# Optimization experiments

Hardware: AMD Instinct MI355X
Metric: run time of the kernel (lower is better)

The kernel has to match this reference:

```python
import jax, jax.numpy as jnp
import numpy as np

HEAD_SIZE = 16  # matches init_kwargs head_size


def _rope_angles(seq_len, half_dim, base=10000.0):
    # standard RoPE frequencies, matches typical precompute_pos_cis
    freqs = 1.0 / (base ** (np.arange(0, half_dim, dtype=np.float32) / half_dim))
    t = np.arange(seq_len, dtype=np.float32)
    ang = np.outer(t, freqs)  # (S, half_dim)
    return jnp.asarray(np.cos(ang)), jnp.asarray(np.sin(ang))


def setup_inputs() -> dict:
    key = jax.random.key(0)
    ks = jax.random.split(key, 10)
    B, S, D = 2, 2048, 1024
    hd = D // HEAD_SIZE
    pos_cos, pos_sin = _rope_angles(S, hd // 2)
    w = lambda k: jax.random.normal(k, (D, D), jnp.float32) * 0.02
    b = lambda k: jax.random.normal(k, (D,), jnp.float32) * 0.02
    return {
        "x": jax.random.normal(ks[0], (B, S, D), jnp.float32),
        "pos_cos": pos_cos,
        "pos_sin": pos_sin,
        "wq_w": w(ks[1]), "wq_b": b(ks[2]),
        "wk_w": w(ks[3]), "wk_b": b(ks[4]),
        "wv_w": w(ks[5]), "wv_b": b(ks[6]),
        "wo_w": w(ks[7]), "wo_b": b(ks[8]),
    }


def _apply_rope(t, cos, sin):
    # t: (B, S, H, hd); cos/sin: (S, hd//2) -> broadcast (1, S, 1, hd//2)
    B, S, H, hd = t.shape
    tr = t.reshape(B, S, H, hd // 2, 2)
    a, b = tr[..., 0], tr[..., 1]
    c = cos[None, :, None, :]
    s = sin[None, :, None, :]
    # complex multiply (a + ib) * (c + is)
    out_r = a * c - b * s
    out_i = a * s + b * c
    return jnp.stack([out_r, out_i], axis=-1).reshape(B, S, H, hd)


def reference(x, pos_cos, pos_sin, wq_w, wq_b, wk_w, wk_b, wv_w, wv_b, wo_w, wo_b):
    B, S, D = x.shape
    H = HEAD_SIZE
    hd = D // H
    q = (x @ wq_w.T + wq_b).reshape(B, S, H, hd)
    k = (x @ wk_w.T + wk_b).reshape(B, S, H, hd)
    v = (x @ wv_w.T + wv_b).reshape(B, S, H, hd)
    q = _apply_rope(q, pos_cos, pos_sin)
    k = _apply_rope(k, pos_cos, pos_sin)
    scale = 1.0 / jnp.sqrt(jnp.asarray(hd, x.dtype))
    scores = jnp.einsum('bshd,bthd->bhst', q, k) * scale  # (B,H,S,S)
    causal = jnp.tril(jnp.ones((S, S), bool))
    scores = jnp.where(causal[None, None], scores, jnp.asarray(-jnp.inf, scores.dtype))
    probs = jax.nn.softmax(scores, axis=-1)
    out = jnp.einsum('bhst,bthd->bshd', probs, v).reshape(B, S, D)
    return out @ wo_w.T + wo_b
```

## Files before the change

### kernel.cpp

```cpp
#include <hip/hip_runtime.h>
#include <stdint.h>
#include <stddef.h>


typedef __bf16 bf16x8 __attribute__((ext_vector_type(8)));
typedef float  f32x4  __attribute__((ext_vector_type(4)));

__device__ __forceinline__ unsigned short f2b(float f) {
  union { float f; uint32_t u; } v; v.f = f;
  uint32_t u = v.u;
  return (unsigned short)((u + 0x7FFFu + ((u >> 16) & 1u)) >> 16);
}

__device__ __forceinline__ void async16(const void* g, void* l) {
  __builtin_amdgcn_global_load_lds(
      (const __attribute__((address_space(1))) void*)g,
      (__attribute__((address_space(3))) void*)l, 16, 0, 0);
}

__global__ void cast_x_tiled_kernel(const float* __restrict__ in,
                                    unsigned short* __restrict__ out) {
  int i = blockIdx.x * blockDim.x + threadIdx.x;
  const int L  = i & 1023;
  const int kt = (i >> 10) & 15;
  const int pn = i >> 14;
  const int row = pn * 128 + ((L >> 7) << 4) + (L & 15);
  const int k0  = kt * 64 + ((L >> 4) & 7) * 8;
  const float4* src = (const float4*)(in + (size_t)row * 1024 + k0);
  float4 a = src[0], b = src[1];
  uint4 pk;
  pk.x = (uint32_t)f2b(a.x) | ((uint32_t)f2b(a.y) << 16);
  pk.y = (uint32_t)f2b(a.z) | ((uint32_t)f2b(a.w) << 16);
  pk.z = (uint32_t)f2b(b.x) | ((uint32_t)f2b(b.y) << 16);
  pk.w = (uint32_t)f2b(b.z) | ((uint32_t)f2b(b.w) << 16);
  *(uint4*)(out + (size_t)i * 8) = pk;
}

__global__ void cast_w_tiled_kernel(const float* __restrict__ wq,
                                    const float* __restrict__ wk,
                                    const float* __restrict__ wv,
                                    unsigned short* __restrict__ out) {
  int i = blockIdx.x * blockDim.x + threadIdx.x;
  const int mat = i >> 17;
  const int rem = i & 131071;
  const int L  = rem & 1023;
  const int kt = (rem >> 10) & 15;
  const int pn = rem >> 14;
  const float* src = (mat == 0) ? wq : (mat == 1) ? wk : wv;
  const int row = pn * 128 + ((L >> 7) << 4) + (L & 15);
  const int k0  = kt * 64 + ((L >> 4) & 7) * 8;
  const float4* s = (const float4*)(src + (size_t)row * 1024 + k0);
  float4 a = s[0], b = s[1];
  uint4 pk;
  pk.x = (uint32_t)f2b(a.x) | ((uint32_t)f2b(a.y) << 16);
  pk.y = (uint32_t)f2b(a.z) | ((uint32_t)f2b(a.w) << 16);
  pk.z = (uint32_t)f2b(b.x) | ((uint32_t)f2b(b.y) << 16);
  pk.w = (uint32_t)f2b(b.z) | ((uint32_t)f2b(b.w) << 16);
  *(uint4*)(out + (size_t)i * 8) = pk;
}

__global__ void cast_kernel(const float* __restrict__ in,
                            unsigned short* __restrict__ out, int n4) {
  int i = blockIdx.x * blockDim.x + threadIdx.x;
  if (i >= n4) return;
  float4 v = ((const float4*)in)[i];
  ushort4 o;
  o.x = f2b(v.x); o.y = f2b(v.y); o.z = f2b(v.z); o.w = f2b(v.w);
  ((ushort4*)out)[i] = o;
}

__global__ __launch_bounds__(256, 3) void qkv_gemm_kernel(
    const unsigned short* __restrict__ A,
    const unsigned short* __restrict__ W,
    const float* __restrict__ biasq, const float* __restrict__ biask,
    const float* __restrict__ biasv,
    const float* __restrict__ cp, const float* __restrict__ sp,
    unsigned short* __restrict__ qo,
    unsigned short* __restrict__ ko,
    unsigned short* __restrict__ vo)
{
  const int tid  = threadIdx.x;
  const int w    = tid >> 6, l = tid & 63;
  const int lm   = l & 15,  quad = l >> 4;
  const int nblk = blockIdx.x;
  const int m0   = blockIdx.y * 128;
  const int wm   = (w >> 1) * 64, wn = (w & 1) * 64;

  const unsigned short* At = A + (size_t)blockIdx.y * 16 * 8192;
  const unsigned short* Wt = W + (size_t)nblk * 16 * 8192;

  const f32x4 fzero = {0.f, 0.f, 0.f, 0.f};
  f32x4 acc[4][4];
#pragma unroll
  for (int i = 0; i < 4; ++i)
#pragma unroll
    for (int j = 0; j < 4; ++j) acc[i][j] = fzero;

  bf16x8 pA[4], pB[4], qA[4], qB[4];

#define QKV_LOADH(DA, DB, T, KK)                                              \
  {                                                                           \
    const unsigned short* Ab_ = At + (size_t)(T) * 8192;                      \
    const unsigned short* Wb_ = Wt + (size_t)(T) * 8192;                      \
    _Pragma("unroll")                                                         \
    for (int i = 0; i < 4; ++i)                                               \
      DA[i] = *(const bf16x8*)(Ab_ +                                          \
          (size_t)((((w >> 1) * 4 + i) * 128 + (KK) * 64 + l)) * 8);          \
    _Pragma("unroll")                                                         \
    for (int j = 0; j < 4; ++j)                                               \
      DB[j] = *(const bf16x8*)(Wb_ +                                          \
          (size_t)((((w & 1) * 4 + j) * 128 + (KK) * 64 + l)) * 8);           \
  }

#define QKV_MFMAH(SA, SB)                                                     \
  _Pragma("unroll")                                                           \
  for (int i = 0; i < 4; ++i)                                                 \
    _Pragma("unroll")                                                         \
    for (int j = 0; j < 4; ++j)                                               \
      acc[i][j] = __builtin_amdgcn_mfma_f32_16x16x32_bf16(SA[i], SB[j],       \
                                                          acc[i][j], 0, 0, 0);

  QKV_LOADH(pA, pB, 0, 0);
#pragma unroll 1
  for (int t = 0; t < 16; ++t) {
    QKV_LOADH(qA, qB, t, 1);
    QKV_MFMAH(pA, pB);
    if (t < 15) QKV_LOADH(pA, pB, t + 1, 0);
    QKV_MFMAH(qA, qB);
  }
#undef QKV_LOADH
#undef QKV_MFMAH

  const int which = nblk >> 3;
  const int n0    = (nblk & 7) * 128;
  const float* bias = (which == 0) ? biasq : (which == 1) ? biask : biasv;
#pragma unroll
  for (int i = 0; i < 4; ++i) {
#pragma unroll
    for (int j = 0; j < 4; ++j) {
      const int n = n0 + wn + j * 16 + lm;
      const float bval = bias[n];
      const int h = n >> 6, d = n & 63;
      float vals[4];
#pragma unroll
      for (int r = 0; r < 4; ++r) {
        const int m = m0 + wm + i * 16 + quad * 4 + r;
        const int srow = m & 2047;
        float val = acc[i][j][r] + bval;
        if (which != 2) {
          const float c  = cp[srow * 32 + (d >> 1)];
          const float sn = sp[srow * 32 + (d >> 1)];
          const float part = __shfl_xor(val, 1, 64);
          val = (d & 1) ? (part * sn + val * c) : (val * c - part * sn);
        }
        vals[r] = val;
      }
      const int mbase = m0 + wm + i * 16 + quad * 4;
      const int b = mbase >> 11, s0 = mbase & 2047;
      const int bh = (b << 4) + h;
      if (which == 0) {
#pragma unroll
        for (int r = 0; r < 4; ++r)
          qo[((size_t)bh * 2048 + s0 + r) * 64 + d] = f2b(vals[r]);
      } else if (which == 1) {
#pragma unroll
        for (int r = 0; r < 4; ++r) {
          const int s = s0 + r;
          ko[((size_t)bh * 32 + (s >> 6)) * 4096 +
             (size_t)(((d >> 3) * 64 + (s & 63))) * 8 + (d & 7)] = f2b(vals[r]);
        }
      } else {
        uint32_t w0 = (uint32_t)f2b(vals[0]) | ((uint32_t)f2b(vals[1]) << 16);
        uint32_t w1 = (uint32_t)f2b(vals[2]) | ((uint32_t)f2b(vals[3]) << 16);
        uint2 pk; pk.x = w0; pk.y = w1;
        *(uint2*)(vo + ((size_t)bh * 32 + (s0 >> 6)) * 4096 +
                  (size_t)((((s0 & 63) >> 3) * 64 + d)) * 8 + (s0 & 7)) = pk;
      }
    }
  }
}

__global__ __launch_bounds__(256, 4) void flash_kernel(
    const unsigned short* __restrict__ Q,
    const unsigned short* __restrict__ K,
    const unsigned short* __restrict__ VT,
    unsigned short* __restrict__ O)
{
  constexpr int PSTRIDE = 72;
  __shared__ unsigned short Ps[64 * PSTRIDE];
  const int tid = threadIdx.x;
  const int w = tid >> 6, l = tid & 63, lm = l & 15, quad = l >> 4;
  const int bh = blockIdx.x, qt = 31 - (int)blockIdx.y;
  const int row0 = qt * 64 + w * 16;

  bf16x8 aq[2];
#pragma unroll
  for (int kc = 0; kc < 2; ++kc)
    aq[kc] = *(const bf16x8*)(Q + ((size_t)bh * 2048 + row0 + lm) * 64 + kc * 32 + quad * 8);

  const f32x4 fzero = {0.f, 0.f, 0.f, 0.f};
  f32x4 Oacc[4];
#pragma unroll
  for (int jo = 0; jo < 4; ++jo) Oacc[jo] = fzero;
  float m_i = -1e30f, l_i = 0.f;

  const int nkv = qt + 1;

#pragma unroll 1
  for (int kt = 0; kt < nkv - 1; ++kt) {
    const size_t tbase = ((size_t)bh * 32 + kt) * 4096;
    bf16x8 kf[2][4], vf[2][4];
#pragma unroll
    for (int kc = 0; kc < 2; ++kc)
#pragma unroll
      for (int tb = 0; tb < 4; ++tb) {
        const size_t off = tbase + (size_t)(((kc * 4 + quad) * 64 + tb * 16 + lm)) * 8;
        kf[kc][tb] = *(const bf16x8*)(K + off);
        vf[kc][tb] = *(const bf16x8*)(VT + off);
      }
    f32x4 Sc[4];
#pragma unroll
    for (int tb = 0; tb < 4; ++tb) Sc[tb] = fzero;
#pragma unroll
    for (int kc = 0; kc < 2; ++kc)
#pragma unroll
      for (int tb = 0; tb < 4; ++tb)
        Sc[tb] = __builtin_amdgcn_mfma_f32_16x16x32_bf16(kf[kc][tb], aq[kc], Sc[tb], 0, 0, 0);

    float mx = -1e30f;
#pragma unroll
    for (int tb = 0; tb < 4; ++tb)
#pragma unroll
      for (int r = 0; r < 4; ++r) {
        float s = Sc[tb][r] * 0.125f;
        Sc[tb][r] = s;
        mx = fmaxf(mx, s);
      }
    mx = fmaxf(mx, __shfl_xor(mx, 16, 64));
    mx = fmaxf(mx, __shfl_xor(mx, 32, 64));

    const bool skip = (bool)__all(mx - m_i <= 8.0f);
    float alpha = 1.f;
    if (!skip) {
      const float mnew = fmaxf(m_i, mx);
      alpha = __expf(m_i - mnew);
      m_i = mnew;
    }
    const float mref = m_i;

    float ps = 0.f;
#pragma unroll
    for (int tb = 0; tb < 4; ++tb) {
      float p0 = __expf(Sc[tb][0] - mref), p1 = __expf(Sc[tb][1] - mref);
      float p2 = __expf(Sc[tb][2] - mref), p3 = __expf(Sc[tb][3] - mref);
      ps += (p0 + p1) + (p2 + p3);
      uint2 pk;
      pk.x = (uint32_t)f2b(p0) | ((uint32_t)f2b(p1) << 16);
      pk.y = (uint32_t)f2b(p2) | ((uint32_t)f2b(p3) << 16);
      *(uint2*)(Ps + (size_t)(w * 16 + lm) * PSTRIDE + tb * 16 + quad * 4) = pk;
    }
    ps += __shfl_xor(ps, 16, 64);
    ps += __shfl_xor(ps, 32, 64);
    if (skip) {
      l_i += ps;
    } else {
      l_i = l_i * alpha + ps;
      float af4[4];
#pragma unroll
      for (int r = 0; r < 4; ++r) af4[r] = __shfl(alpha, quad * 4 + r, 64);
#pragma unroll
      for (int jo = 0; jo < 4; ++jo)
#pragma unroll
        for (int r = 0; r < 4; ++r) Oacc[jo][r] *= af4[r];
    }

#pragma unroll
    for (int kc = 0; kc < 2; ++kc) {
      bf16x8 ap = *(const bf16x8*)(Ps + (size_t)(w * 16 + lm) * PSTRIDE + kc * 32 + quad * 8);
#pragma unroll
      for (int jo = 0; jo < 4; ++jo)
        Oacc[jo] = __builtin_amdgcn_mfma_f32_16x16x32_bf16(ap, vf[kc][jo], Oacc[jo], 0, 0, 0);
    }
  }

  {
    const size_t tbase = ((size_t)bh * 32 + qt) * 4096;
    bf16x8 kf[2][4], vf[2][4];
#pragma unroll
    for (int kc = 0; kc < 2; ++kc)
#pragma unroll
      for (int tb = 0; tb < 4; ++tb) {
        const size_t off = tbase + (size_t)(((kc * 4 + quad) * 64 + tb * 16 + lm)) * 8;
        kf[kc][tb] = *(const bf16x8*)(K + off);
        vf[kc][tb] = *(const bf16x8*)(VT + off);
      }
    f32x4 Sc[4];
#pragma unroll
    for (int tb = 0; tb < 4; ++tb) Sc[tb] = fzero;
#pragma unroll
    for (int kc = 0; kc < 2; ++kc)
#pragma unroll
      for (int tb = 0; tb < 4; ++tb)
        Sc[tb] = __builtin_amdgcn_mfma_f32_16x16x32_bf16(kf[kc][tb], aq[kc], Sc[tb], 0, 0, 0);

    const int mrel = w * 16 + lm;
    float mx = -1e30f;
#pragma unroll
    for (int tb = 0; tb < 4; ++tb)
#pragma unroll
      for (int r = 0; r < 4; ++r) {
        float s = Sc[tb][r] * 0.125f;
        if (tb * 16 + quad * 4 + r > mrel) s = -1e30f;
        Sc[tb][r] = s;
        mx = fmaxf(mx, s);
      }
    mx = fmaxf(mx, __shfl_xor(mx, 16, 64));
    mx = fmaxf(mx, __shfl_xor(mx, 32, 64));
    const float mnew  = fmaxf(m_i, mx);
    const float alpha = __expf(m_i - mnew);
    m_i = mnew;

    float ps = 0.f;
#pragma unroll
    for (int tb = 0; tb < 4; ++tb) {
      float p0 = __expf(Sc[tb][0] - mnew), p1 = __expf(Sc[tb][1] - mnew);
      float p2 = __expf(Sc[tb][2] - mnew), p3 = __expf(Sc[tb][3] - mnew);
      ps += (p0 + p1) + (p2 + p3);
      uint2 pk;
      pk.x = (uint32_t)f2b(p0) | ((uint32_t)f2b(p1) << 16);
      pk.y = (uint32_t)f2b(p2) | ((uint32_t)f2b(p3) << 16);
      *(uint2*)(Ps + (size_t)(w * 16 + lm) * PSTRIDE + tb * 16 + quad * 4) = pk;
    }
    ps += __shfl_xor(ps, 16, 64);
    ps += __shfl_xor(ps, 32, 64);
    l_i = l_i * alpha + ps;

    float af4[4];
#pragma unroll
    for (int r = 0; r < 4; ++r) af4[r] = __shfl(alpha, quad * 4 + r, 64);
#pragma unroll
    for (int jo = 0; jo < 4; ++jo)
#pragma unroll
      for (int r = 0; r < 4; ++r) Oacc[jo][r] *= af4[r];

#pragma unroll
    for (int kc = 0; kc < 2; ++kc) {
      bf16x8 ap = *(const bf16x8*)(Ps + (size_t)(w * 16 + lm) * PSTRIDE + kc * 32 + quad * 8);
#pragma unroll
      for (int jo = 0; jo < 4; ++jo)
        Oacc[jo] = __builtin_amdgcn_mfma_f32_16x16x32_bf16(ap, vf[kc][jo], Oacc[jo], 0, 0, 0);
    }
  }

  float lf[4];
#pragma unroll
  for (int r = 0; r < 4; ++r) lf[r] = 1.0f / __shfl(l_i, quad * 4 + r, 64);
  const int b = bh >> 4, h = bh & 15;
#pragma unroll
  for (int jo = 0; jo < 4; ++jo)
#pragma unroll
    for (int r = 0; r < 4; ++r) {
      const int s   = row0 + quad * 4 + r;
      const int col = h * 64 + jo * 16 + lm;
      O[((size_t)b * 2048 + s) * 1024 + col] = f2b(Oacc[jo][r] * lf[r]);
    }
}

__global__ __launch_bounds__(256) void oproj_gemm_kernel(
    const unsigned short* __restrict__ A,
    const unsigned short* __restrict__ W,
    const float* __restrict__ bias,
    float* __restrict__ out)
{
  __shared__ unsigned short As[64 * 64];
  __shared__ unsigned short Bs[128 * 64];
  const int tid = threadIdx.x;
  const int w = tid >> 6, l = tid & 63;
  const int lm = l & 15, quad = l >> 4;
  const int m0 = blockIdx.y * 64;
  const int n0 = blockIdx.x * 128;

  const f32x4 fzero = {0.f, 0.f, 0.f, 0.f};
  f32x4 acc[4][2];
#pragma unroll
  for (int i = 0; i < 4; ++i)
#pragma unroll
    for (int j = 0; j < 2; ++j) acc[i][j] = fzero;

  for (int k0 = 0; k0 < 1024; k0 += 64) {
    __syncthreads();
#pragma unroll
    for (int q = 0; q < 2; ++q) {
      const int row = w * 16 + lm;
      const int kc  = quad + 4 * q;
      async16(A + (size_t)(m0 + row) * 1024 + k0 + kc * 8,
              As + ((size_t)w * 128 + 64 * q) * 8);
    }
#pragma unroll
    for (int q = 0; q < 4; ++q) {
      const int row = w * 16 + lm + (q & 1) * 64;
      const int kc  = quad + 4 * (q >> 1);
      async16(W + (size_t)(n0 + row) * 1024 + k0 + kc * 8,
              Bs + ((size_t)(w + 4 * (q & 1)) * 128 + 64 * (q >> 1)) * 8);
    }
    __syncthreads();
#pragma unroll
    for (int kk = 0; kk < 2; ++kk) {
      bf16x8 af[4], bfc[2];
#pragma unroll
      for (int i = 0; i < 4; ++i)
        af[i] = *(const bf16x8*)(As + (size_t)((i * 128 + kk * 64 + l)) * 8);
#pragma unroll
      for (int j = 0; j < 2; ++j)
        bfc[j] = *(const bf16x8*)(Bs + (size_t)(((w * 2 + j) * 128 + kk * 64 + l)) * 8);
#pragma unroll
      for (int i = 0; i < 4; ++i)
#pragma unroll
        for (int j = 0; j < 2; ++j)
          acc[i][j] = __builtin_amdgcn_mfma_f32_16x16x32_bf16(af[i], bfc[j], acc[i][j], 0, 0, 0);
    }
  }

#pragma unroll
  for (int i = 0; i < 4; ++i) {
#pragma unroll
    for (int j = 0; j < 2; ++j) {
      const int n = n0 + w * 32 + j * 16 + lm;
      const float bval = bias[n];
#pragma unroll
      for (int r = 0; r < 4; ++r) {
        const int m = m0 + i * 16 + quad * 4 + r;
        out[(size_t)m * 1024 + n] = acc[i][j][r] + bval;
      }
    }
  }
}

extern "C" void kernel_launch(void* const* d_in, const int* in_sizes, int n_in,
                              void* d_out, int out_size, void* d_ws, size_t ws_size,
                              hipStream_t stream) {
  (void)in_sizes; (void)n_in; (void)out_size; (void)ws_size;
  const float* x  = (const float*)d_in[0];
  const float* cp = (const float*)d_in[1];
  const float* sp = (const float*)d_in[2];
  const float* wq = (const float*)d_in[3];
  const float* bq = (const float*)d_in[4];
  const float* wk = (const float*)d_in[5];
  const float* bk = (const float*)d_in[6];
  const float* wv = (const float*)d_in[7];
  const float* bv = (const float*)d_in[8];
  const float* wo = (const float*)d_in[9];
  const float* bo = (const float*)d_in[10];
  float* out = (float*)d_out;

  unsigned short* xbf  = (unsigned short*)d_ws;
  unsigned short* wqkv = xbf  + (size_t)4 * 1024 * 1024;
  unsigned short* wobf = wqkv + (size_t)3 * 1024 * 1024;
  unsigned short* qbf  = wobf + (size_t)1 * 1024 * 1024;
  unsigned short* kbf  = qbf  + (size_t)4 * 1024 * 1024;
  unsigned short* vbf  = kbf  + (size_t)4 * 1024 * 1024;
  unsigned short* obf  = vbf  + (size_t)4 * 1024 * 1024;

  hipLaunchKernelGGL(cast_x_tiled_kernel, dim3(2048), dim3(256), 0, stream, x, xbf);
  hipLaunchKernelGGL(cast_w_tiled_kernel, dim3(1536), dim3(256), 0, stream,
                     wq, wk, wv, wqkv);
  hipLaunchKernelGGL(cast_kernel, dim3(1024), dim3(256), 0, stream, wo, wobf, 262144);

  hipLaunchKernelGGL(qkv_gemm_kernel, dim3(24, 32), dim3(256), 0, stream,
                     xbf, wqkv, bq, bk, bv, cp, sp, qbf, kbf, vbf);
  hipLaunchKernelGGL(flash_kernel, dim3(32, 32), dim3(256), 0, stream,
                     qbf, kbf, vbf, obf);
  hipLaunchKernelGGL(oproj_gemm_kernel, dim3(8, 64), dim3(256), 0, stream,
                     obf, wobf, bo, out);
}
```

Measured before the change: 209.8 us.

## Fuse casts into one kernel and feed o-proj from pre-tiled layouts via registers

The three cast kernels are merged into one launch that writes x and all four weight matrices in an MFMA-fragment tiled layout. The flash kernel now stores its output in the same tiled layout, so the output-projection GEMM can load fragments straight from global memory into registers. That GEMM drops LDS staging and barriers and double-buffers its register loads across k-steps. The intent is fewer launches and no LDS round-trips or syncs, at the cost of the flash kernel's scattered 2-byte stores and loads that reach global memory without LDS reuse.

```diff
diff --git a/kernel.cpp b/kernel.cpp
--- a/kernel.cpp
+++ b/kernel.cpp
@@ -12,41 +12,33 @@
   return (unsigned short)((u + 0x7FFFu + ((u >> 16) & 1u)) >> 16);
 }
 
-__device__ __forceinline__ void async16(const void* g, void* l) {
-  __builtin_amdgcn_global_load_lds(
-      (const __attribute__((address_space(1))) void*)g,
-      (__attribute__((address_space(3))) void*)l, 16, 0, 0);
-}
-
-__global__ void cast_x_tiled_kernel(const float* __restrict__ in,
-                                    unsigned short* __restrict__ out) {
+__global__ void cast_all_kernel(const float* __restrict__ x,
+                                const float* __restrict__ wq,
+                                const float* __restrict__ wk,
+                                const float* __restrict__ wv,
+                                const float* __restrict__ wo,
+                                unsigned short* __restrict__ xbf,
+                                unsigned short* __restrict__ wqkv,
+                                unsigned short* __restrict__ wobf) {
   int i = blockIdx.x * blockDim.x + threadIdx.x;
-  const int L  = i & 1023;
-  const int kt = (i >> 10) & 15;
-  const int pn = i >> 14;
-  const int row = pn * 128 + ((L >> 7) << 4) + (L & 15);
-  const int k0  = kt * 64 + ((L >> 4) & 7) * 8;
-  const float4* src = (const float4*)(in + (size_t)row * 1024 + k0);
-  float4 a = src[0], b = src[1];
-  uint4 pk;
-  pk.x = (uint32_t)f2b(a.x) | ((uint32_t)f2b(a.y) << 16);
-  pk.y = (uint32_t)f2b(a.z) | ((uint32_t)f2b(a.w) << 16);
-  pk.z = (uint32_t)f2b(b.x) | ((uint32_t)f2b(b.y) << 16);
-  pk.w = (uint32_t)f2b(b.z) | ((uint32_t)f2b(b.w) << 16);
-  *(uint4*)(out + (size_t)i * 8) = pk;
-}
-
-__global__ void cast_w_tiled_kernel(const float* __restrict__ wq,
-                                    const float* __restrict__ wk,
-                                    const float* __restrict__ wv,
-                                    unsigned short* __restrict__ out) {
-  int i = blockIdx.x * blockDim.x + threadIdx.x;
-  const int mat = i >> 17;
-  const int rem = i & 131071;
-  const int L  = rem & 1023;
-  const int kt = (rem >> 10) & 15;
-  const int pn = rem >> 14;
-  const float* src = (mat == 0) ? wq : (mat == 1) ? wk : wv;
+  const float* src;
+  unsigned short* dst;
+  int rem;
+  if (i < 524288) {
+    src = x; dst = xbf; rem = i;
+  } else if (i < 917504) {
+    rem = i - 524288;
+    const int mat = rem >> 17;
+    src = (mat == 0) ? wq : (mat == 1) ? wk : wv;
+    dst = wqkv;
+  } else {
+    rem = i - 917504;
+    src = wo; dst = wobf;
+  }
+  const int inmat = (i < 524288) ? rem : (i < 917504) ? (rem & 131071) : rem;
+  const int L  = inmat & 1023;
+  const int kt = (inmat >> 10) & 15;
+  const int pn = inmat >> 14;
   const int row = pn * 128 + ((L >> 7) << 4) + (L & 15);
   const int k0  = kt * 64 + ((L >> 4) & 7) * 8;
   const float4* s = (const float4*)(src + (size_t)row * 1024 + k0);
@@ -56,17 +48,10 @@
   pk.y = (uint32_t)f2b(a.z) | ((uint32_t)f2b(a.w) << 16);
   pk.z = (uint32_t)f2b(b.x) | ((uint32_t)f2b(b.y) << 16);
   pk.w = (uint32_t)f2b(b.z) | ((uint32_t)f2b(b.w) << 16);
-  *(uint4*)(out + (size_t)i * 8) = pk;
-}
-
-__global__ void cast_kernel(const float* __restrict__ in,
-                            unsigned short* __restrict__ out, int n4) {
-  int i = blockIdx.x * blockDim.x + threadIdx.x;
-  if (i >= n4) return;
-  float4 v = ((const float4*)in)[i];
-  ushort4 o;
-  o.x = f2b(v.x); o.y = f2b(v.y); o.z = f2b(v.z); o.w = f2b(v.w);
-  ((ushort4*)out)[i] = o;
+  const size_t oidx = (i < 524288) ? (size_t)rem
+                    : (i < 917504) ? (size_t)rem
+                    : (size_t)rem;
+  *(uint4*)(dst + oidx * 8) = pk;
 }
 
 __global__ __launch_bounds__(256, 3) void qkv_gemm_kernel(
@@ -356,29 +341,32 @@
 #pragma unroll
   for (int r = 0; r < 4; ++r) lf[r] = 1.0f / __shfl(l_i, quad * 4 + r, 64);
   const int b = bh >> 4, h = bh & 15;
-#pragma unroll
-  for (int jo = 0; jo < 4; ++jo)
-#pragma unroll
-    for (int r = 0; r < 4; ++r) {
-      const int s   = row0 + quad * 4 + r;
-      const int col = h * 64 + jo * 16 + lm;
-      O[((size_t)b * 2048 + s) * 1024 + col] = f2b(Oacc[jo][r] * lf[r]);
-    }
-}
-
-__global__ __launch_bounds__(256) void oproj_gemm_kernel(
+  const size_t obase = ((size_t)((b * 16 + (qt >> 1)) * 16 + h)) * 8192;
+  const int Lbase = ((qt & 1) * 4 + w) * 128 + quad * 4;
+#pragma unroll
+  for (int jo = 0; jo < 4; ++jo) {
+    const int Ljo = Lbase + (jo * 2 + (lm >> 3)) * 16;
+#pragma unroll
+    for (int r = 0; r < 4; ++r)
+      O[obase + (size_t)(Ljo + r) * 8 + (lm & 7)] = f2b(Oacc[jo][r] * lf[r]);
+  }
+}
+
+__global__ __launch_bounds__(256, 2) void oproj_gemm_kernel(
     const unsigned short* __restrict__ A,
     const unsigned short* __restrict__ W,
     const float* __restrict__ bias,
     float* __restrict__ out)
 {
-  __shared__ unsigned short As[64 * 64];
-  __shared__ unsigned short Bs[128 * 64];
   const int tid = threadIdx.x;
   const int w = tid >> 6, l = tid & 63;
   const int lm = l & 15, quad = l >> 4;
+  const int nblk = blockIdx.x;
   const int m0 = blockIdx.y * 64;
-  const int n0 = blockIdx.x * 128;
+  const int half = blockIdx.y & 1;
+
+  const unsigned short* At = A + (size_t)(blockIdx.y >> 1) * 16 * 8192;
+  const unsigned short* Wt = W + (size_t)nblk * 16 * 8192;
 
   const f32x4 fzero = {0.f, 0.f, 0.f, 0.f};
   f32x4 acc[4][2];
@@ -387,45 +375,46 @@
 #pragma unroll
     for (int j = 0; j < 2; ++j) acc[i][j] = fzero;
 
-  for (int k0 = 0; k0 < 1024; k0 += 64) {
-    __syncthreads();
-#pragma unroll
-    for (int q = 0; q < 2; ++q) {
-      const int row = w * 16 + lm;
-      const int kc  = quad + 4 * q;
-      async16(A + (size_t)(m0 + row) * 1024 + k0 + kc * 8,
-              As + ((size_t)w * 128 + 64 * q) * 8);
-    }
-#pragma unroll
-    for (int q = 0; q < 4; ++q) {
-      const int row = w * 16 + lm + (q & 1) * 64;
-      const int kc  = quad + 4 * (q >> 1);
-      async16(W + (size_t)(n0 + row) * 1024 + k0 + kc * 8,
-              Bs + ((size_t)(w + 4 * (q & 1)) * 128 + 64 * (q >> 1)) * 8);
-    }
-    __syncthreads();
-#pragma unroll
-    for (int kk = 0; kk < 2; ++kk) {
-      bf16x8 af[4], bfc[2];
-#pragma unroll
-      for (int i = 0; i < 4; ++i)
-        af[i] = *(const bf16x8*)(As + (size_t)((i * 128 + kk * 64 + l)) * 8);
-#pragma unroll
-      for (int j = 0; j < 2; ++j)
-        bfc[j] = *(const bf16x8*)(Bs + (size_t)(((w * 2 + j) * 128 + kk * 64 + l)) * 8);
-#pragma unroll
-      for (int i = 0; i < 4; ++i)
-#pragma unroll
-        for (int j = 0; j < 2; ++j)
-          acc[i][j] = __builtin_amdgcn_mfma_f32_16x16x32_bf16(af[i], bfc[j], acc[i][j], 0, 0, 0);
-    }
-  }
+  bf16x8 pA[4], pB[2], qA[4], qB[2];
+
+#define OP_LOADH(DA, DB, T, KK)                                               \
+  {                                                                           \
+    const unsigned short* Ab_ = At + (size_t)(T) * 8192;                      \
+    const unsigned short* Wb_ = Wt + (size_t)(T) * 8192;                      \
+    _Pragma("unroll")                                                         \
+    for (int i = 0; i < 4; ++i)                                               \
+      DA[i] = *(const bf16x8*)(Ab_ +                                          \
+          (size_t)(((half * 4 + i) * 128 + (KK) * 64 + l)) * 8);              \
+    _Pragma("unroll")                                                         \
+    for (int j = 0; j < 2; ++j)                                               \
+      DB[j] = *(const bf16x8*)(Wb_ +                                          \
+          (size_t)(((w * 2 + j) * 128 + (KK) * 64 + l)) * 8);                 \
+  }
+
+#define OP_MFMAH(SA, SB)                                                      \
+  _Pragma("unroll")                                                           \
+  for (int i = 0; i < 4; ++i)                                                 \
+    _Pragma("unroll")                                                         \
+    for (int j = 0; j < 2; ++j)                                               \
+      acc[i][j] = __builtin_amdgcn_mfma_f32_16x16x32_bf16(SA[i], SB[j],       \
+                                                          acc[i][j], 0, 0, 0);
+
+  OP_LOADH(pA, pB, 0, 0);
+#pragma unroll 1
+  for (int t = 0; t < 16; ++t) {
+    OP_LOADH(qA, qB, t, 1);
+    OP_MFMAH(pA, pB);
+    if (t < 15) OP_LOADH(pA, pB, t + 1, 0);
+    OP_MFMAH(qA, qB);
+  }
+#undef OP_LOADH
+#undef OP_MFMAH
 
 #pragma unroll
   for (int i = 0; i < 4; ++i) {
 #pragma unroll
     for (int j = 0; j < 2; ++j) {
-      const int n = n0 + w * 32 + j * 16 + lm;
+      const int n = nblk * 128 + w * 32 + j * 16 + lm;
       const float bval = bias[n];
 #pragma unroll
       for (int r = 0; r < 4; ++r) {
@@ -461,10 +450,8 @@
   unsigned short* vbf  = kbf  + (size_t)4 * 1024 * 1024;
   unsigned short* obf  = vbf  + (size_t)4 * 1024 * 1024;
 
-  hipLaunchKernelGGL(cast_x_tiled_kernel, dim3(2048), dim3(256), 0, stream, x, xbf);
-  hipLaunchKernelGGL(cast_w_tiled_kernel, dim3(1536), dim3(256), 0, stream,
-                     wq, wk, wv, wqkv);
-  hipLaunchKernelGGL(cast_kernel, dim3(1024), dim3(256), 0, stream, wo, wobf, 262144);
+  hipLaunchKernelGGL(cast_all_kernel, dim3(4096), dim3(256), 0, stream,
+                     x, wq, wk, wv, wo, xbf, wqkv, wobf);
 
   hipLaunchKernelGGL(qkv_gemm_kernel, dim3(24, 32), dim3(256), 0, stream,
                      xbf, wqkv, bq, bk, bv, cp, sp, qbf, kbf, vbf);
```

New measurement: 200.3 us. 4.5% less time.
